# Kernel optimization log

Hardware: AMD Instinct MI355X
Metric: run time of the kernel (lower is better)

The kernel has to match this reference:

```python
import jax, jax.numpy as jnp
import numpy as np
import math

# static config (see shape_source)
NUM_GRAPHS = 8      # b
L_NODES = 1024      # nodes per graph (uniform -> to_dense_batch is a reshape)
D_INNER = 128
HEADDIM = 16
N_HEADS = D_INNER // HEADDIM  # 8
D_STATE = 64
NUM_DT = 4          # 3 node-dt components + dt_self
AVG_DEG = 16
DIAMETER = 50       # default_graph_diameter
TOL = 0.1
DT_MIN, DT_MAX, DT_FLOOR = 1e-3, 1e-1, 1e-4


def dag_inverse(A):
    """DAGInverse.forward: (I - A)^{-1} via repeated-squaring doubling.
    A: [b, h, l, l]. j = 2^ceil(log2(diameter)); out = prod (I + A^{2^k})."""
    j = 2 ** math.ceil(math.log2(DIAMETER))  # 64
    I = jnp.eye(A.shape[-1], dtype=A.dtype)
    last = A
    out = I + A
    for _ in range(2, int(math.log2(j)) + 1):  # 5 iterations
        last = last @ last
        out = out @ (I + last)
    return out


def setup_inputs() -> dict:
    key = jax.random.key(0)
    k = jax.random.split(key, 8)
    N = NUM_GRAPHS * L_NODES
    x = jax.random.normal(k[0], (N, D_INNER), jnp.float32)
    B_mat = jax.random.normal(k[1], (N, D_STATE), jnp.float32)
    C_mat = jax.random.normal(k[2], (N, D_STATE), jnp.float32)
    dt = jax.random.normal(k[3], (N, NUM_DT * N_HEADS), jnp.float32)
    # dt_bias init as in GraphSSD.__init__
    u = jax.random.uniform(k[4], (N_HEADS,), jnp.float32)
    dt0 = jnp.exp(u * (math.log(DT_MAX) - math.log(DT_MIN)) + math.log(DT_MIN))
    dt0 = jnp.clip(dt0, DT_FLOOR, None)
    dt_bias = dt0 + jnp.log(-jnp.expm1(-dt0))
    D = jnp.ones((N_HEADS,), jnp.float32)
    # edges: per-graph random endpoints, offset to global node ids
    E_per = L_NODES * AVG_DEG
    src_l = jax.random.randint(k[5], (NUM_GRAPHS, E_per), 0, L_NODES)
    dst_l = jax.random.randint(k[6], (NUM_GRAPHS, E_per), 0, L_NODES)
    off = (jnp.arange(NUM_GRAPHS) * L_NODES)[:, None]
    edge_index = jnp.stack([(src_l + off).reshape(-1), (dst_l + off).reshape(-1)], 0).astype(jnp.int32)
    return {"x": x, "B_mat": B_mat, "C_mat": C_mat, "dt": dt,
            "dt_bias": dt_bias, "D": D, "edge_index": edge_index}


def reference(x, B_mat, C_mat, dt, dt_bias, D, edge_index):
    Bn, Lg, H, hd, ds = NUM_GRAPHS, L_NODES, N_HEADS, HEADDIM, D_STATE
    N = Bn * Lg
    # dense batching (uniform graph sizes -> pure reshape, mask all True)
    x_d = x.reshape(Bn, Lg, H, hd).transpose(0, 2, 1, 3)        # b n l h ('(n h)' split)
    B_d = B_mat.reshape(Bn, Lg, ds)                             # broadcast over heads
    C_d = C_mat.reshape(Bn, Lg, ds)
    # dt: 'l (n c) -> c n l'
    dt_c = dt.reshape(N, H, NUM_DT).transpose(2, 1, 0)          # c n l
    dt_node, dt_self = dt_c[:NUM_DT - 1], dt_c[NUM_DT - 1]      # (3,n,N), (n,N)
    dt_self_d = dt_self.T.reshape(Bn, Lg, H).transpose(0, 2, 1)  # b n l
    # multiply_dt_w_A: A = -exp(A_log)= -1 (with_A=False)
    dt_A_node = -jax.nn.softplus(dt_node + dt_bias[None, :, None])  # (3, n, N)
    # edge dt: (dt_s[src] + dt_t[dst]) / 2, then exp
    src, dst = edge_index[0], edge_index[1]
    attr = jnp.exp((dt_A_node[0][:, src] + dt_A_node[1][:, dst]) * 0.5).T  # (E, n)
    # to_dense_adj scatter: [b, l1, l2, h] then -> b h l1 l2
    b_idx, sl, dl = src // Lg, src % Lg, dst % Lg
    A_mat = jnp.zeros((Bn, Lg, Lg, H), x.dtype).at[b_idx, sl, dl].add(attr)
    A_mat = A_mat.transpose(0, 3, 1, 2)                          # b n l1 l2
    # 'leq' normalization with dummy self term
    dt_dummy = jnp.exp(dt_A_node[2]).T.reshape(Bn, Lg, H).transpose(0, 2, 1)  # b n l
    normalizer = A_mat.sum(-1) + dt_dummy                        # b n l1
    A_norm = A_mat / (normalizer[..., None] + TOL)
    # L = (I - A^T)^{-1} via DAGInverse doubling
    Lmat = dag_inverse(jnp.swapaxes(A_norm, -1, -2).astype(jnp.float32))  # b n l t
    L_norm = Lmat * dt_self_d[:, :, None, :]                     # scale along t
    # y = einsum(C, L, B, x); C/B broadcast in heads -> G shared across heads
    G = jnp.einsum('bld,btd->blt', C_d, B_d)[:, None]            # b 1 l t
    y = jnp.einsum('bnlt,bnth->bnlh', L_norm * G, x_d)
    y = y + x_d * D[None, :, None, None]
    # 'b n l h -> b l (h n)'
    y = y.transpose(0, 2, 3, 1).reshape(Bn, Lg, H * hd)
    return y.reshape(N, H * hd)
```

## Files before the change

kernel.cpp:

```cpp
#include <hip/hip_runtime.h>
#include <hip/hip_bf16.h>

#define H_ 8
#define NTOT 8192
#define LG 1024
#define BN 8
#define HD 16
#define DSTATE 64
#define EPG 16384
#define MSZ (1024*1024)

typedef __hip_bfloat16 bf16;
typedef unsigned short ushort_t;
typedef _Float16 f16;
typedef __attribute__((ext_vector_type(8))) _Float16 half8;
typedef __attribute__((ext_vector_type(4))) _Float16 half4;
typedef __attribute__((ext_vector_type(4))) float f4v;

__device__ __forceinline__ float b2f(bf16 v){ return __bfloat162float(v); }
__device__ __forceinline__ float sp_(float z){
  return fmaxf(z, 0.f) + log1pf(expf(-fabsf(z)));
}
__device__ __forceinline__ float ldv(const void* p, size_t i, int f32){
  float v;
  if (f32) v = ((const float*)p)[i];
  else     v = b2f(((const bf16*)p)[i]);
  return v;
}
__device__ __forceinline__ void gl2lds16(const void* g, void* l){
  __builtin_amdgcn_global_load_lds((const __attribute__((address_space(1))) unsigned int*)g,
                                   (__attribute__((address_space(3))) unsigned int*)l,
                                   16, 0, 0);
}
__device__ __forceinline__ unsigned ldsaddr(const void* p){
  return (unsigned)(uintptr_t)(__attribute__((address_space(3))) const char*)p;
}

#define BARC() do { asm volatile("" ::: "memory"); __builtin_amdgcn_s_barrier(); asm volatile("" ::: "memory"); } while(0)
#define SB0() __builtin_amdgcn_sched_barrier(0)
#define DSR(dst, base, off) asm volatile("ds_read_b128 %0, %1 offset:" #off : "=v"(dst) : "v"(base))

__global__ void k_sniff(const void* __restrict__ dt, int* __restrict__ flag){
  const ushort_t* p = (const ushort_t*)dt;
  int tid = threadIdx.x;
  int bad = 0;
  for (int i = tid; i < 512; i += 256){
    int e = (p[i] >> 7) & 0xFF;
    if (e >= 140) bad = 1;
  }
  unsigned long long m = __ballot(bad != 0);
  __shared__ int anybad[4];
  if ((tid & 63) == 0) anybad[tid >> 6] = (m != 0ull) ? 1 : 0;
  __syncthreads();
  if (tid == 0) *flag = (anybad[0] | anybad[1] | anybad[2] | anybad[3]);
}

__global__ void k_nodecoef(const void* __restrict__ dt, const void* __restrict__ dtb,
                           const int* __restrict__ flag,
                           float* __restrict__ a0, float* __restrict__ a1,
                           float* __restrict__ dum, float* __restrict__ sdt){
  int idx = blockIdx.x*256 + threadIdx.x;
  if (idx >= H_*NTOT) return;
  int f32 = *flag;
  int h = idx / NTOT, n = idx - h*NTOT;
  float bias = ldv(dtb, h, f32);
  size_t base = (size_t)n*(4*H_) + h*4;
  float d0, d1, d2, d3;
  if (f32){
    const float* row = (const float*)dt + base;
    d0 = row[0]; d1 = row[1]; d2 = row[2]; d3 = row[3];
  } else {
    const bf16* row = (const bf16*)dt + base;
    d0 = b2f(row[0]); d1 = b2f(row[1]); d2 = b2f(row[2]); d3 = b2f(row[3]);
  }
  a0[(size_t)n*H_ + h] = -sp_(d0 + bias);
  a1[(size_t)n*H_ + h] = -sp_(d1 + bias);
  dum[idx] = expf(-sp_(d2 + bias));
  sdt[idx] = d3;
}

__global__ __launch_bounds__(256) void k_zero(char* base, size_t regB, float* __restrict__ nrm){
  int bh = blockIdx.y;
  if (blockIdx.x < 1024){
    float* Mf = (float*)(base + (size_t)bh*regB) + MSZ;
    int i = blockIdx.x*1024 + threadIdx.x*4;
    *(float4*)(Mf + i) = make_float4(0.f,0.f,0.f,0.f);
  } else {
    int j = threadIdx.x*4;
    *(float4*)(nrm + (size_t)bh*LG + j) = make_float4(0.f,0.f,0.f,0.f);
  }
}

__global__ void k_scatter(const int* __restrict__ ei, const float* __restrict__ a0,
                          const float* __restrict__ a1, char* base, size_t regB,
                          float* __restrict__ nrm,
                          int b0, int h0, int lgHB, int GBp, int nthreads, int Etot){
  int t = blockIdx.x*256 + threadIdx.x;
  if (t >= nthreads) return;
  int HB = 1 << lgHB;
  int hl = t & (HB-1);
  int el = t >> lgHB;
  int e = b0*EPG + el;
  int src = ei[e], dst = ei[Etot + e];
  int g = src >> 10;
  if ((unsigned)(g - b0) >= (unsigned)GBp) return;
  int sl = src & 1023, dl = dst & 1023;
  int h = h0 + hl;
  float attr = expf(0.5f*(a0[(size_t)src*H_ + h] + a1[(size_t)dst*H_ + h]));
  int bhl = (g - b0)*HB + hl;
  float* Mf = (float*)(base + (size_t)bhl*regB) + MSZ;
  atomicAdd(&Mf[(size_t)dl*LG + sl], attr);
  atomicAdd(&nrm[bhl*LG + sl], attr);
}

__global__ __launch_bounds__(256) void k_norm2(char* base, size_t regB,
                            const float* __restrict__ nrm, const float* __restrict__ dum,
                            int b0, int h0, int HB){
  __shared__ ushort_t tb[32][33];
  int bh = blockIdx.z;
  int g = b0 + bh / HB, h = h0 + bh % HB;
  const float* Mf = (const float*)(base + (size_t)bh*regB) + MSZ;
  f16* L0  = (f16*)(base + (size_t)bh*regB);
  f16* L0T = L0 + MSZ;
  f16* O0  = L0 + (size_t)4*MSZ;
  int x0 = blockIdx.x*32, y0 = blockIdx.y*32;
  int tx = threadIdx.x & 31, ty = threadIdx.x >> 5;
  int sl = x0 + tx;
  float denom = nrm[(size_t)bh*LG + sl] + dum[(size_t)h*NTOT + g*LG + sl] + 0.1f;
  float rden = 1.f / denom;
  #pragma unroll
  for (int i = 0; i < 32; i += 8){
    int dl = y0 + ty + i;
    float v = Mf[(size_t)dl*LG + sl] * rden;
    f16 hv = (f16)v;
    L0[(size_t)dl*LG + sl] = hv;
    O0[(size_t)dl*LG + sl] = (f16)(v + (dl == sl ? 1.f : 0.f));
    union { f16 h; ushort_t u; } cv; cv.h = hv;
    tb[tx][ty + i] = cv.u;
  }
  __syncthreads();
  #pragma unroll
  for (int i = 0; i < 32; i += 8){
    union { f16 h; ushort_t u; } cv; cv.u = tb[ty + i][tx];
    L0T[(size_t)(x0 + ty + i)*LG + y0 + tx] = cv.h;
  }
}

__global__ __launch_bounds__(256) void k_G(const void* __restrict__ Bm, const void* __restrict__ Cm,
                                           const int* __restrict__ flag,
                                           f16* __restrict__ G, int b0){
  int gl = blockIdx.z;
  int g = b0 + gl;
  int l0 = blockIdx.y*16, t0 = blockIdx.x*16;
  __shared__ float Cs[16][DSTATE+1];
  __shared__ float Bs[16][DSTATE+1];
  int tid = threadIdx.x;
  int f32 = *flag;
  if (f32){
    const float* Cf = (const float*)Cm;
    const float* Bf = (const float*)Bm;
    for (int i = tid; i < 16*DSTATE; i += 256){
      int r = i >> 6, d = i & 63;
      Cs[r][d] = Cf[(size_t)(g*LG + l0 + r)*DSTATE + d];
      Bs[r][d] = Bf[(size_t)(g*LG + t0 + r)*DSTATE + d];
    }
  } else {
    const bf16* Cb = (const bf16*)Cm;
    const bf16* Bb = (const bf16*)Bm;
    for (int i = tid; i < 16*DSTATE; i += 256){
      int r = i >> 6, d = i & 63;
      Cs[r][d] = b2f(Cb[(size_t)(g*LG + l0 + r)*DSTATE + d]);
      Bs[r][d] = b2f(Bb[(size_t)(g*LG + t0 + r)*DSTATE + d]);
    }
  }
  __syncthreads();
  int r = tid >> 4, c = tid & 15;
  float acc = 0.f;
  #pragma unroll
  for (int d = 0; d < DSTATE; ++d) acc = fmaf(Cs[r][d], Bs[c][d], acc);
  G[(size_t)gl*MSZ + (size_t)(l0+r)*LG + t0 + c] = (f16)acc;
}

__global__ __launch_bounds__(512, 4) void k_gemm_fused(char* base, size_t regB,
    int nS, int iAs, int iBTs, int iCs, int iCTs,
    int nU, int iAu, int iBTu, int iCu){
  extern __shared__ char lds[];
  int T = nS + nU;
  int s = blockIdx.x + 8*blockIdx.z;
  if (s >= T) return;
  int isS = (s < nS) ? 1 : 0;
  int bh  = isS ? s : (s - nS);
  int iA  = isS ? iAs : iAu;
  int iBT = isS ? iBTs : iBTu;
  int iC  = isS ? iCs : iCu;
  int iCT = isS ? iCTs : -1;
  int addA = 1 - isS;
  char* reg = base + (size_t)bh*regB;
  const f16* Ab = (const f16*)reg + (size_t)iA*MSZ;
  const f16* Bb = (const f16*)reg + (size_t)iBT*MSZ;
  f16* Cb = (f16*)reg + (size_t)iC*MSZ;
  int y = blockIdx.y;
  int i0 = (y >> 2)*128, j0 = (y & 3)*256;
  int tid = threadIdx.x;
  int lane = tid & 63, wv = tid >> 6;
  int wm = wv >> 2, wn = wv & 3;
  int m16 = lane & 15, q = lane >> 4;
  int swz = (q ^ ((m16 >> 1) & 3)) << 4;
  int aoff = ((wm << 6) + m16)*64 + swz;
  int boff = ((wn << 6) + m16)*64 + swz;
  int sra = tid >> 2;
  int sca = (tid & 3) ^ ((sra >> 1) & 3);
  int idx1 = tid + 512;
  int srb1 = idx1 >> 2;
  int scb1 = (idx1 & 3) ^ ((srb1 >> 1) & 3);

  auto ISSUE = [&](int tk){
    if (tk >= 32) return;
    char* sl = lds + (size_t)(tk % 3)*24576;
    const f16* As = Ab + (size_t)(i0 + sra)*LG + tk*32 + sca*8;
    gl2lds16(As, sl + tid*16);
    const f16* Bs0 = Bb + (size_t)(j0 + sra)*LG + tk*32 + sca*8;
    gl2lds16(Bs0, sl + 8192 + tid*16);
    const f16* Bs1 = Bb + (size_t)(j0 + srb1)*LG + tk*32 + scb1*8;
    gl2lds16(Bs1, sl + 8192 + (size_t)idx1*16);
  };
  unsigned lbase = ldsaddr(lds);
  auto ADDRA = [&](int tk){ return lbase + (unsigned)((tk % 3)*24576) + (unsigned)aoff; };
  auto ADDRB = [&](int tk){ return lbase + (unsigned)((tk % 3)*24576 + 8192) + (unsigned)boff; };

  #define READ8(tk) do { \
    unsigned aA = ADDRA(tk), aB = ADDRB(tk); \
    DSR(bf0, aB, 0); DSR(bf1, aB, 1024); DSR(bf2, aB, 2048); DSR(bf3, aB, 3072); \
    DSR(af0, aA, 0); DSR(af1, aA, 1024); DSR(af2, aA, 2048); DSR(af3, aA, 3072); } while(0)
  #define MFMA16() do { \
    acc[0][0] = __builtin_amdgcn_mfma_f32_16x16x32_f16(af0, bf0, acc[0][0], 0, 0, 0); \
    acc[0][1] = __builtin_amdgcn_mfma_f32_16x16x32_f16(af0, bf1, acc[0][1], 0, 0, 0); \
    acc[0][2] = __builtin_amdgcn_mfma_f32_16x16x32_f16(af0, bf2, acc[0][2], 0, 0, 0); \
    acc[0][3] = __builtin_amdgcn_mfma_f32_16x16x32_f16(af0, bf3, acc[0][3], 0, 0, 0); \
    acc[1][0] = __builtin_amdgcn_mfma_f32_16x16x32_f16(af1, bf0, acc[1][0], 0, 0, 0); \
    acc[1][1] = __builtin_amdgcn_mfma_f32_16x16x32_f16(af1, bf1, acc[1][1], 0, 0, 0); \
    acc[1][2] = __builtin_amdgcn_mfma_f32_16x16x32_f16(af1, bf2, acc[1][2], 0, 0, 0); \
    acc[1][3] = __builtin_amdgcn_mfma_f32_16x16x32_f16(af1, bf3, acc[1][3], 0, 0, 0); \
    acc[2][0] = __builtin_amdgcn_mfma_f32_16x16x32_f16(af2, bf0, acc[2][0], 0, 0, 0); \
    acc[2][1] = __builtin_amdgcn_mfma_f32_16x16x32_f16(af2, bf1, acc[2][1], 0, 0, 0); \
    acc[2][2] = __builtin_amdgcn_mfma_f32_16x16x32_f16(af2, bf2, acc[2][2], 0, 0, 0); \
    acc[2][3] = __builtin_amdgcn_mfma_f32_16x16x32_f16(af2, bf3, acc[2][3], 0, 0, 0); \
    acc[3][0] = __builtin_amdgcn_mfma_f32_16x16x32_f16(af3, bf0, acc[3][0], 0, 0, 0); \
    acc[3][1] = __builtin_amdgcn_mfma_f32_16x16x32_f16(af3, bf1, acc[3][1], 0, 0, 0); \
    acc[3][2] = __builtin_amdgcn_mfma_f32_16x16x32_f16(af3, bf2, acc[3][2], 0, 0, 0); \
    acc[3][3] = __builtin_amdgcn_mfma_f32_16x16x32_f16(af3, bf3, acc[3][3], 0, 0, 0); } while(0)

  ISSUE(0); ISSUE(1);
  f4v acc[4][4] = {};
  half8 af0, af1, af2, af3, bf0, bf1, bf2, bf3;
  asm volatile("s_waitcnt vmcnt(3)" ::: "memory");
  BARC();

  for (int kt = 0; kt < 32; ++kt){
    READ8(kt);
    ISSUE(kt + 2);
    asm volatile("s_waitcnt lgkmcnt(0)"); SB0();
    __builtin_amdgcn_s_setprio(1);
    MFMA16();
    __builtin_amdgcn_s_setprio(0);
    if (kt < 30)       asm volatile("s_waitcnt vmcnt(3)" ::: "memory");
    else if (kt == 30) asm volatile("s_waitcnt vmcnt(0)" ::: "memory");
    BARC();
  }
  #undef READ8
  #undef MFMA16

  f16* CT = (f16*)reg + (size_t)((iCT < 0) ? iC : iCT)*MSZ;
  #pragma unroll
  for (int mt = 0; mt < 4; ++mt){
    #pragma unroll
    for (int nt = 0; nt < 4; ++nt){
      int gr0 = i0 + wm*64 + mt*16 + q*4;
      int gc  = j0 + wn*64 + nt*16 + m16;
      half4 tv;
      #pragma unroll
      for (int r = 0; r < 4; ++r){
        float v = acc[mt][nt][r];
        if (addA) v += (float)Ab[(size_t)(gr0 + r)*LG + gc];
        f16 hv = (f16)v;
        tv[r] = hv;
        Cb[(size_t)(gr0 + r)*LG + gc] = hv;
      }
      if (iCT >= 0)
        *(half4*)&CT[(size_t)gc*LG + gr0] = tv;
    }
  }
}

__global__ __launch_bounds__(256) void k_final2(char* base, size_t regB, int iO,
    const f16* __restrict__ Gh, const float* __restrict__ sdt,
    const void* __restrict__ x, const void* __restrict__ Dv,
    const int* __restrict__ flag, void* __restrict__ out,
    int b0, int h0, int HB){
  __shared__ float coef[16][257];
  int bh = blockIdx.y;
  int gl = bh / HB, g = b0 + gl, h = h0 + bh % HB;
  int L0r = blockIdx.x*16;
  int tid = threadIdx.x;
  int lr = tid >> 4, ts = tid & 15;
  int f32 = *flag;
  const f16* Orow = (const f16*)(base + (size_t)bh*regB) + (size_t)iO*MSZ + (size_t)(L0r+lr)*LG;
  const f16* Grow = Gh + (size_t)gl*MSZ + (size_t)(L0r+lr)*LG;
  const float* srow = sdt + (size_t)h*NTOT + g*LG;
  float acc = 0.f;
  for (int tc = 0; tc < LG; tc += 256){
    int tb = tc + ts*16;
    __syncthreads();
    half8 o0 = *(const half8*)&Orow[tb];
    half8 o1 = *(const half8*)&Orow[tb + 8];
    half8 g0 = *(const half8*)&Grow[tb];
    half8 g1 = *(const half8*)&Grow[tb + 8];
    #pragma unroll
    for (int j = 0; j < 8; ++j){
      coef[lr][ts*16 + j]     = (float)o0[j] * (float)g0[j] * srow[tb + j];
      coef[lr][ts*16 + 8 + j] = (float)o1[j] * (float)g1[j] * srow[tb + 8 + j];
    }
    __syncthreads();
    if (f32){
      const float* xf = (const float*)x + (size_t)(g*LG + tc)*128 + h*HD + ts;
      for (int t = 0; t < 256; ++t)
        acc = fmaf(coef[lr][t], xf[(size_t)t*128], acc);
    } else {
      const bf16* xb = (const bf16*)x + (size_t)(g*LG + tc)*128 + h*HD + ts;
      for (int t = 0; t < 256; ++t)
        acc = fmaf(coef[lr][t], b2f(xb[(size_t)t*128]), acc);
    }
  }
  int l = L0r + lr, d = ts;
  float xs = ldv(x, (size_t)(g*LG + l)*128 + h*HD + d, f32);
  float dv = ldv(Dv, h, f32);
  float v = acc + xs*dv;
  size_t off = (size_t)(g*LG + l)*128 + d*H_ + h;
  if (f32) ((float*)out)[off] = v;
  else     ((bf16*)out)[off] = __float2bfloat16(v);
}

extern "C" void kernel_launch(void* const* d_in, const int* in_sizes, int n_in,
                              void* d_out, int out_size, void* d_ws, size_t ws_size,
                              hipStream_t stream){
  const void* x   = d_in[0];
  const void* Bm  = d_in[1];
  const void* Cm  = d_in[2];
  const void* dt  = d_in[3];
  const void* dtb = d_in[4];
  const void* Dv  = d_in[5];
  const int*  ei  = (const int*)d_in[6];
  int Etot = in_sizes[6] / 2;

  static int attrDone = 0;
  if (!attrDone){
    hipFuncSetAttribute(reinterpret_cast<const void*>(k_gemm_fused),
                        hipFuncAttributeMaxDynamicSharedMemorySize, 131072);
    attrDone = 1;
  }

  const size_t REG = (size_t)6*MSZ*2;
  int GB = 1, HB = 1;
  const int cfgs[7][2] = {{8,8},{4,8},{2,8},{1,8},{1,4},{1,2},{1,1}};
  for (int i = 0; i < 7; ++i){
    int gb = cfgs[i][0], hb = cfgs[i][1];
    size_t need = 4ull*(4ull*H_*NTOT + 64)
                + 4ull*(size_t)gb*hb*LG
                + 2ull*(size_t)gb*MSZ
                + (size_t)gb*hb*REG;
    if (need <= ws_size){ GB = gb; HB = hb; break; }
  }
  int lgHB = (HB==8)?3:((HB==4)?2:((HB==2)?1:0));
  int nbh = GB*HB;

  float* a0  = (float*)d_ws;
  float* a1  = a0 + H_*NTOT;
  float* dum = a1 + H_*NTOT;
  float* sdt = dum + H_*NTOT;
  int*  flag = (int*)(sdt + H_*NTOT);
  float* nrm = (float*)flag + 64;
  f16* G     = (f16*)(nrm + (size_t)nbh*LG);
  char* chainBase = (char*)(G + (size_t)GB*MSZ);

  k_sniff<<<1, 256, 0, stream>>>(dt, flag);
  k_nodecoef<<<(H_*NTOT + 255)/256, 256, 0, stream>>>(dt, dtb, flag, a0, a1, dum, sdt);

  for (int b0 = 0; b0 < BN; b0 += GB){
    for (int h0 = 0; h0 < H_; h0 += HB){
      k_zero<<<dim3(1025, nbh), 256, 0, stream>>>(chainBase, REG, nrm);
      int nthr = GB*EPG*HB;
      k_scatter<<<(nthr + 255)/256, 256, 0, stream>>>(ei, a0, a1, chainBase, REG, nrm,
                                                      b0, h0, lgHB, GB, nthr, Etot);
      k_norm2<<<dim3(32, 32, nbh), 256, 0, stream>>>(chainBase, REG, nrm, dum, b0, h0, HB);
      if (h0 == 0){
        dim3 gg(64, 64, GB);
        k_G<<<gg, 256, 0, stream>>>(Bm, Cm, flag, G, b0);
      }
      int lA = 0, lAT = 1, lC = 2, lCT = 3, oA = 4, oC = 5;
      {
        int T = nbh;
        dim3 gg(8, 32, (T + 7)/8);
        k_gemm_fused<<<gg, 512, 73728, stream>>>(chainBase, REG, nbh, lA, lAT, lC, lCT,
                                                 0, 0, 0, 0);
      }
      for (int k = 0; k < 4; ++k){
        int T = 2*nbh;
        dim3 gg(8, 32, (T + 7)/8);
        k_gemm_fused<<<gg, 512, 73728, stream>>>(chainBase, REG,
                                                 nbh, lC, lCT, lA, lAT,
                                                 nbh, oA, lCT, oC);
        int tp;
        tp = lA; lA = lC; lC = tp;
        tp = lAT; lAT = lCT; lCT = tp;
        tp = oA; oA = oC; oC = tp;
      }
      {
        int T = nbh;
        dim3 gg(8, 32, (T + 7)/8);
        k_gemm_fused<<<gg, 512, 73728, stream>>>(chainBase, REG, 0, 0, 0, 0, 0,
                                                 nbh, oA, lCT, oC);
        int tp = oA; oA = oC; oC = tp;
      }
      dim3 fg(64, nbh);
      k_final2<<<fg, 256, 0, stream>>>(chainBase, REG, oA, G, sdt, x, Dv, flag, d_out, b0, h0, HB);
    }
  }
}
```

Before: 2.369 ms.

## Deepen GEMM pipeline to four LDS stages with register double-buffered fragments

The fused fp16 GEMM main loop is restructured from a 3-slot LDS ring, where each iteration reads fragments and then issues MFMAs, into a 4-slot ring unrolled by four. Two register fragment sets alternate so that LDS reads for the next k-step overlap the current MFMA block, and global prefetch runs three tiles ahead. Global addresses become pointer increments instead of being recomputed each step. In exchange, dynamic LDS grows from 72KB to 96KB and launch bounds drop to 2 blocks per CU, which may reduce occupancy and latency hiding across waves.

```diff
diff --git a/kernel.cpp b/kernel.cpp
--- a/kernel.cpp
+++ b/kernel.cpp
@@ -27,11 +27,6 @@
   else     v = b2f(((const bf16*)p)[i]);
   return v;
 }
-__device__ __forceinline__ void gl2lds16(const void* g, void* l){
-  __builtin_amdgcn_global_load_lds((const __attribute__((address_space(1))) unsigned int*)g,
-                                   (__attribute__((address_space(3))) unsigned int*)l,
-                                   16, 0, 0);
-}
 __device__ __forceinline__ unsigned ldsaddr(const void* p){
   return (unsigned)(uintptr_t)(__attribute__((address_space(3))) const char*)p;
 }
@@ -39,6 +34,8 @@
 #define BARC() do { asm volatile("" ::: "memory"); __builtin_amdgcn_s_barrier(); asm volatile("" ::: "memory"); } while(0)
 #define SB0() __builtin_amdgcn_sched_barrier(0)
 #define DSR(dst, base, off) asm volatile("ds_read_b128 %0, %1 offset:" #off : "=v"(dst) : "v"(base))
+#define GLD(p, d) __builtin_amdgcn_global_load_lds((const __attribute__((address_space(1))) unsigned int*)(p), \
+    (__attribute__((address_space(3))) unsigned int*)(d), 16, 0, 0)
 
 __global__ void k_sniff(const void* __restrict__ dt, int* __restrict__ flag){
   const ushort_t* p = (const ushort_t*)dt;
@@ -181,7 +178,33 @@
   G[(size_t)gl*MSZ + (size_t)(l0+r)*LG + t0 + c] = (f16)acc;
 }
 
-__global__ __launch_bounds__(512, 4) void k_gemm_fused(char* base, size_t regB,
+#define RD_S0(s) do{ \
+  DSR(af##s##0,aAlo,0);     DSR(af##s##1,aAlo,1024);  DSR(af##s##2,aAlo,2048);  DSR(af##s##3,aAlo,3072); \
+  DSR(bf##s##0,aBlo,0);     DSR(bf##s##1,aBlo,1024);  DSR(bf##s##2,aBlo,2048);  DSR(bf##s##3,aBlo,3072); }while(0)
+#define RD_S1(s) do{ \
+  DSR(af##s##0,aAlo,24576); DSR(af##s##1,aAlo,25600); DSR(af##s##2,aAlo,26624); DSR(af##s##3,aAlo,27648); \
+  DSR(bf##s##0,aBlo,24576); DSR(bf##s##1,aBlo,25600); DSR(bf##s##2,aBlo,26624); DSR(bf##s##3,aBlo,27648); }while(0)
+#define RD_S2(s) do{ \
+  DSR(af##s##0,aAhi,0);     DSR(af##s##1,aAhi,1024);  DSR(af##s##2,aAhi,2048);  DSR(af##s##3,aAhi,3072); \
+  DSR(bf##s##0,aBhi,0);     DSR(bf##s##1,aBhi,1024);  DSR(bf##s##2,aBhi,2048);  DSR(bf##s##3,aBhi,3072); }while(0)
+#define RD_S3(s) do{ \
+  DSR(af##s##0,aAhi,24576); DSR(af##s##1,aAhi,25600); DSR(af##s##2,aAhi,26624); DSR(af##s##3,aAhi,27648); \
+  DSR(bf##s##0,aBhi,24576); DSR(bf##s##1,aBhi,25600); DSR(bf##s##2,aBhi,26624); DSR(bf##s##3,aBhi,27648); }while(0)
+#define MF1(s, m, n) acc[m][n] = __builtin_amdgcn_mfma_f32_16x16x32_f16(af##s##m, bf##s##n, acc[m][n], 0, 0, 0)
+#define MFMA16(s) do{ \
+  MF1(s,0,0); MF1(s,0,1); MF1(s,0,2); MF1(s,0,3); \
+  MF1(s,1,0); MF1(s,1,1); MF1(s,1,2); MF1(s,1,3); \
+  MF1(s,2,0); MF1(s,2,1); MF1(s,2,2); MF1(s,2,3); \
+  MF1(s,3,0); MF1(s,3,1); MF1(s,3,2); MF1(s,3,3); }while(0)
+#define ISS(SL, GOFF) do{ \
+  GLD(pA  + (GOFF), dA  + (SL)); \
+  GLD(pB0 + (GOFF), dB0 + (SL)); \
+  GLD(pB1 + (GOFF), dB1 + (SL)); }while(0)
+#define LGKM0() asm volatile("s_waitcnt lgkmcnt(0)" ::: "memory")
+#define VM3()   asm volatile("s_waitcnt vmcnt(3)" ::: "memory")
+#define VM0()   asm volatile("s_waitcnt vmcnt(0)" ::: "memory")
+
+__global__ __launch_bounds__(512, 2) void k_gemm_fused(char* base, size_t regB,
     int nS, int iAs, int iBTs, int iCs, int iCTs,
     int nU, int iAu, int iBTu, int iCu){
   extern __shared__ char lds[];
@@ -205,70 +228,57 @@
   int lane = tid & 63, wv = tid >> 6;
   int wm = wv >> 2, wn = wv & 3;
   int m16 = lane & 15, q = lane >> 4;
-  int swz = (q ^ ((m16 >> 1) & 3)) << 4;
-  int aoff = ((wm << 6) + m16)*64 + swz;
-  int boff = ((wn << 6) + m16)*64 + swz;
-  int sra = tid >> 2;
-  int sca = (tid & 3) ^ ((sra >> 1) & 3);
-  int idx1 = tid + 512;
-  int srb1 = idx1 >> 2;
-  int scb1 = (idx1 & 3) ^ ((srb1 >> 1) & 3);
-
-  auto ISSUE = [&](int tk){
-    if (tk >= 32) return;
-    char* sl = lds + (size_t)(tk % 3)*24576;
-    const f16* As = Ab + (size_t)(i0 + sra)*LG + tk*32 + sca*8;
-    gl2lds16(As, sl + tid*16);
-    const f16* Bs0 = Bb + (size_t)(j0 + sra)*LG + tk*32 + sca*8;
-    gl2lds16(Bs0, sl + 8192 + tid*16);
-    const f16* Bs1 = Bb + (size_t)(j0 + srb1)*LG + tk*32 + scb1*8;
-    gl2lds16(Bs1, sl + 8192 + (size_t)idx1*16);
-  };
+  unsigned swz = (unsigned)((q ^ ((m16 >> 1) & 3)) << 4);
   unsigned lbase = ldsaddr(lds);
-  auto ADDRA = [&](int tk){ return lbase + (unsigned)((tk % 3)*24576) + (unsigned)aoff; };
-  auto ADDRB = [&](int tk){ return lbase + (unsigned)((tk % 3)*24576 + 8192) + (unsigned)boff; };
-
-  #define READ8(tk) do { \
-    unsigned aA = ADDRA(tk), aB = ADDRB(tk); \
-    DSR(bf0, aB, 0); DSR(bf1, aB, 1024); DSR(bf2, aB, 2048); DSR(bf3, aB, 3072); \
-    DSR(af0, aA, 0); DSR(af1, aA, 1024); DSR(af2, aA, 2048); DSR(af3, aA, 3072); } while(0)
-  #define MFMA16() do { \
-    acc[0][0] = __builtin_amdgcn_mfma_f32_16x16x32_f16(af0, bf0, acc[0][0], 0, 0, 0); \
-    acc[0][1] = __builtin_amdgcn_mfma_f32_16x16x32_f16(af0, bf1, acc[0][1], 0, 0, 0); \
-    acc[0][2] = __builtin_amdgcn_mfma_f32_16x16x32_f16(af0, bf2, acc[0][2], 0, 0, 0); \
-    acc[0][3] = __builtin_amdgcn_mfma_f32_16x16x32_f16(af0, bf3, acc[0][3], 0, 0, 0); \
-    acc[1][0] = __builtin_amdgcn_mfma_f32_16x16x32_f16(af1, bf0, acc[1][0], 0, 0, 0); \
-    acc[1][1] = __builtin_amdgcn_mfma_f32_16x16x32_f16(af1, bf1, acc[1][1], 0, 0, 0); \
-    acc[1][2] = __builtin_amdgcn_mfma_f32_16x16x32_f16(af1, bf2, acc[1][2], 0, 0, 0); \
-    acc[1][3] = __builtin_amdgcn_mfma_f32_16x16x32_f16(af1, bf3, acc[1][3], 0, 0, 0); \
-    acc[2][0] = __builtin_amdgcn_mfma_f32_16x16x32_f16(af2, bf0, acc[2][0], 0, 0, 0); \
-    acc[2][1] = __builtin_amdgcn_mfma_f32_16x16x32_f16(af2, bf1, acc[2][1], 0, 0, 0); \
-    acc[2][2] = __builtin_amdgcn_mfma_f32_16x16x32_f16(af2, bf2, acc[2][2], 0, 0, 0); \
-    acc[2][3] = __builtin_amdgcn_mfma_f32_16x16x32_f16(af2, bf3, acc[2][3], 0, 0, 0); \
-    acc[3][0] = __builtin_amdgcn_mfma_f32_16x16x32_f16(af3, bf0, acc[3][0], 0, 0, 0); \
-    acc[3][1] = __builtin_amdgcn_mfma_f32_16x16x32_f16(af3, bf1, acc[3][1], 0, 0, 0); \
-    acc[3][2] = __builtin_amdgcn_mfma_f32_16x16x32_f16(af3, bf2, acc[3][2], 0, 0, 0); \
-    acc[3][3] = __builtin_amdgcn_mfma_f32_16x16x32_f16(af3, bf3, acc[3][3], 0, 0, 0); } while(0)
-
-  ISSUE(0); ISSUE(1);
+  unsigned aAlo = lbase + (unsigned)((wm*64 + m16)*64) + swz;
+  unsigned aBlo = lbase + 8192u + (unsigned)((wn*64 + m16)*64) + swz;
+  unsigned aAhi = aAlo + 49152u;
+  unsigned aBhi = aBlo + 49152u;
+  int rs = tid >> 2;
+  int cs = (tid & 3) ^ ((rs >> 1) & 3);
+  const char* pA  = (const char*)(Ab + (size_t)(i0 + rs)*LG + cs*8);
+  const char* pB0 = (const char*)(Bb + (size_t)(j0 + rs)*LG + cs*8);
+  const char* pB1 = (const char*)(Bb + (size_t)(j0 + 128 + rs)*LG + cs*8);
+  char* dA  = lds + (size_t)tid*16;
+  char* dB0 = lds + 8192 + (size_t)tid*16;
+  char* dB1 = lds + 16384 + (size_t)tid*16;
+
   f4v acc[4][4] = {};
-  half8 af0, af1, af2, af3, bf0, bf1, bf2, bf3;
-  asm volatile("s_waitcnt vmcnt(3)" ::: "memory");
+  half8 af00, af01, af02, af03, bf00, bf01, bf02, bf03;
+  half8 af10, af11, af12, af13, bf10, bf11, bf12, bf13;
+
+  ISS(0, 0); ISS(24576, 64); ISS(49152, 128);
+  asm volatile("s_waitcnt vmcnt(6)" ::: "memory");
   BARC();
-
-  for (int kt = 0; kt < 32; ++kt){
-    READ8(kt);
-    ISSUE(kt + 2);
-    asm volatile("s_waitcnt lgkmcnt(0)"); SB0();
-    __builtin_amdgcn_s_setprio(1);
-    MFMA16();
-    __builtin_amdgcn_s_setprio(0);
-    if (kt < 30)       asm volatile("s_waitcnt vmcnt(3)" ::: "memory");
-    else if (kt == 30) asm volatile("s_waitcnt vmcnt(0)" ::: "memory");
-    BARC();
-  }
-  #undef READ8
-  #undef MFMA16
+  RD_S0(0);
+  asm volatile("s_waitcnt lgkmcnt(0) vmcnt(3)" ::: "memory");
+  BARC();
+
+  for (int kt = 0; kt < 28; kt += 4){
+    RD_S1(1); ISS(73728, 192); SB0();
+    __builtin_amdgcn_s_setprio(1); MFMA16(0); __builtin_amdgcn_s_setprio(0); SB0();
+    LGKM0(); VM3(); BARC();
+    RD_S2(0); ISS(0, 256); SB0();
+    __builtin_amdgcn_s_setprio(1); MFMA16(1); __builtin_amdgcn_s_setprio(0); SB0();
+    LGKM0(); VM3(); BARC();
+    RD_S3(1); ISS(24576, 320); SB0();
+    __builtin_amdgcn_s_setprio(1); MFMA16(0); __builtin_amdgcn_s_setprio(0); SB0();
+    LGKM0(); VM3(); BARC();
+    RD_S0(0); ISS(49152, 384); SB0();
+    __builtin_amdgcn_s_setprio(1); MFMA16(1); __builtin_amdgcn_s_setprio(0); SB0();
+    LGKM0(); VM3(); BARC();
+    pA += 256; pB0 += 256; pB1 += 256;
+  }
+  RD_S1(1); ISS(73728, 192); SB0();
+  __builtin_amdgcn_s_setprio(1); MFMA16(0); __builtin_amdgcn_s_setprio(0); SB0();
+  LGKM0(); VM3(); BARC();
+  RD_S2(0); SB0();
+  __builtin_amdgcn_s_setprio(1); MFMA16(1); __builtin_amdgcn_s_setprio(0); SB0();
+  LGKM0(); VM0(); BARC();
+  RD_S3(1); SB0();
+  __builtin_amdgcn_s_setprio(1); MFMA16(0); __builtin_amdgcn_s_setprio(0); SB0();
+  LGKM0(); BARC();
+  __builtin_amdgcn_s_setprio(1); MFMA16(1); __builtin_amdgcn_s_setprio(0);
 
   f16* CT = (f16*)reg + (size_t)((iCT < 0) ? iC : iCT)*MSZ;
   #pragma unroll
@@ -400,13 +410,13 @@
       {
         int T = nbh;
         dim3 gg(8, 32, (T + 7)/8);
-        k_gemm_fused<<<gg, 512, 73728, stream>>>(chainBase, REG, nbh, lA, lAT, lC, lCT,
+        k_gemm_fused<<<gg, 512, 98304, stream>>>(chainBase, REG, nbh, lA, lAT, lC, lCT,
                                                  0, 0, 0, 0);
       }
       for (int k = 0; k < 4; ++k){
         int T = 2*nbh;
         dim3 gg(8, 32, (T + 7)/8);
-        k_gemm_fused<<<gg, 512, 73728, stream>>>(chainBase, REG,
+        k_gemm_fused<<<gg, 512, 98304, stream>>>(chainBase, REG,
                                                  nbh, lC, lCT, lA, lAT,
                                                  nbh, oA, lCT, oC);
         int tp;
@@ -417,7 +427,7 @@
       {
         int T = nbh;
         dim3 gg(8, 32, (T + 7)/8);
-        k_gemm_fused<<<gg, 512, 73728, stream>>>(chainBase, REG, 0, 0, 0, 0, 0,
+        k_gemm_fused<<<gg, 512, 98304, stream>>>(chainBase, REG, 0, 0, 0, 0, 0,
                                                  nbh, oA, lCT, oC);
         int tp = oA; oA = oC; oC = tp;
       }
```

Result: slower. 2.625 ms (+10.8%).
